# Optimization experiments

Measured on AMD Instinct MI355X. Metric: run time of the kernel, lower is better.

The kernel has to match this reference:

```python
import jax, jax.numpy as jnp
import numpy as np

B, C, H, W = 16, 16, 256, 256
HID, OUT_C, IN_C = 128, 13, 3

_SOBEL_X = np.array([[-1, 0, 1], [-2, 0, 2], [-1, 0, 1]], dtype=np.float32)
_SOBEL_Y = _SOBEL_X.T


def setup_inputs() -> dict:
    key = jax.random.key(0)
    k1, k2, k3, k4 = jax.random.split(key, 4)
    return {
        "input_grid": jax.random.normal(k1, (B, C, H, W), dtype=jnp.float32),
        "w1": jax.random.normal(k2, (HID, 3 * C), dtype=jnp.float32) * 0.0001,
        "b1": jax.random.normal(k3, (HID,), dtype=jnp.float32) * 0.0001,
        "w2": jax.random.normal(k4, (OUT_C, HID), dtype=jnp.float32) * 0.0001,
    }


def _depthwise_sobel(x_padded, filt2d):
    # x_padded: [B, C, H+2, W+2]; depthwise 3x3 valid conv (groups=C)
    c = x_padded.shape[1]
    kern = jnp.broadcast_to(jnp.asarray(filt2d)[None, None], (c, 1, 3, 3))
    return jax.lax.conv_general_dilated(
        x_padded, kern, window_strides=(1, 1), padding="VALID",
        feature_group_count=c,
        dimension_numbers=("NCHW", "OIHW", "NCHW"))


def reference(input_grid, w1, b1, w2):
    # circular pad by 1 on spatial dims
    xp = jnp.pad(input_grid, ((0, 0), (0, 0), (1, 1), (1, 1)), mode="wrap")
    gx = _depthwise_sobel(xp, _SOBEL_X)
    gy = _depthwise_sobel(xp, _SOBEL_Y)
    # perception grid: [B, 3C, H, W]
    perception = jnp.concatenate([input_grid, gx, gy], axis=1)
    # update network: 1x1 conv -> ReLU -> 1x1 conv (dropout = identity in eval)
    h = jax.nn.relu(jnp.einsum("bchw,oc->bohw", perception, w1)
                    + b1[None, :, None, None])
    ds = jnp.einsum("bchw,oc->bohw", h, w2)  # [B, C-IN_C, H, W]
    # residual add to channels 3: of the state
    return input_grid.at[:, IN_C:].add(ds)
```

## Files before the change

kernel.cpp:

```cpp
#include <hip/hip_runtime.h>

#define BB   16
#define CC   16
#define HH   256
#define WW   256
#define HID  128
#define OUTC 13

typedef short short8 __attribute__((ext_vector_type(8)));
typedef float floatx16 __attribute__((ext_vector_type(16)));

__device__ __forceinline__ unsigned short f2bf(float x) {
    unsigned int u = __float_as_uint(x);
    u += 0x7fffu + ((u >> 16) & 1u);
    return (unsigned short)(u >> 16);
}

#define W1F_BYTES 36864
#define W2F_OFF   36864

__global__ __launch_bounds__(256) void gca_prep(
    const float* __restrict__ w1, const float* __restrict__ w2,
    unsigned char* __restrict__ ws)
{
    const int id = blockIdx.x * 256 + threadIdx.x;
    const float SX[9] = {-1.f, 0.f, 1.f, -2.f, 0.f, 2.f, -1.f, 0.f, 1.f};
    const float SY[9] = {-1.f, -2.f, -1.f, 0.f, 0.f, 0.f, 1.f, 2.f, 1.f};

    if (id < 2304) {
        const int mtG  = id / 576;
        const int rem  = id % 576;
        const int tap  = rem / 64;
        const int lane = rem % 64;
        const int p  = lane & 31, hi = lane >> 5;
        const int hid = 32 * mtG + p;
        const float cen = (tap == 4) ? 1.f : 0.f;
        const float sxv = SX[tap], syv = SY[tap];
        const float* wr = w1 + hid * 48;
        unsigned int o[4];
        for (int k = 0; k < 4; ++k) {
            int c0 = 8 * hi + 2 * k;
            float v0 = wr[c0]     * cen + wr[16 + c0]     * sxv + wr[32 + c0]     * syv;
            float v1 = wr[c0 + 1] * cen + wr[16 + c0 + 1] * sxv + wr[32 + c0 + 1] * syv;
            o[k] = (unsigned int)f2bf(v0) | ((unsigned int)f2bf(v1) << 16);
        }
        *(uint4*)(ws + (size_t)id * 16) = make_uint4(o[0], o[1], o[2], o[3]);
    } else if (id < 2816) {
        const int id2 = id - 2304;
        const int s    = id2 / 64;
        const int lane = id2 % 64;
        const int outc = lane & 31, hi = lane >> 5;
        unsigned int o[4];
        for (int k = 0; k < 4; ++k) {
            int hid0 = 16 * s + 8 * hi + 2 * k;
            float v0 = (outc < OUTC) ? w2[outc * HID + hid0]     : 0.f;
            float v1 = (outc < OUTC) ? w2[outc * HID + hid0 + 1] : 0.f;
            o[k] = (unsigned int)f2bf(v0) | ((unsigned int)f2bf(v1) << 16);
        }
        *(uint4*)(ws + W2F_OFF + (size_t)id2 * 16) = make_uint4(o[0], o[1], o[2], o[3]);
    }
}

#define TILE_DW 6120
#define CBUF_DW 2304

__global__ __launch_bounds__(256) void gca_main(
    const float* __restrict__ in,
    const float* __restrict__ b1,
    const unsigned char* __restrict__ ws,
    float* __restrict__ out)
{
    __shared__ unsigned int lds[TILE_DW + CBUF_DW];

    const int tid  = threadIdx.x;
    const int wid  = tid >> 6;
    const int lane = tid & 63;
    const int hw   = wid & 1;
    const int P    = wid >> 1;
    const int p    = lane & 31;
    const int hi   = lane >> 5;

    const int bI = blockIdx.x >> 7;
    const int rm = blockIdx.x & 127;
    const int y0 = (rm >> 3) << 4;
    const int x0 = (rm & 7)  << 5;

    {
        unsigned short* tus = (unsigned short*)lds;
        const float* inb = in + ((size_t)bI << 20);
        for (int i = tid; i < 16 * 18 * 34; i += 256) {
            int c   = i / 612;
            int rem = i % 612;
            int row = rem / 34;
            int col = rem % 34;
            int y = (y0 + row - 1) & 255;
            int x = (x0 + col - 1) & 255;
            float v = inb[(c << 16) + (y << 8) + x];
            tus[(row * 34 + col) * 20 + c] = f2bf(v);
        }
    }
    __syncthreads();

    const unsigned char* w1f = ws + ((size_t)(2 * hw) * 9) * 64 * 16;
    const unsigned char* w2f = ws + W2F_OFF + (size_t)(4 * hw) * 64 * 16;
    const int cb = TILE_DW + P * (64 * 18) + lane * 18;

#pragma unroll 1
    for (int t = 0; t < 8; ++t) {
        const int row = y0 + 2 * t + P;

        floatx16 acc1[2];
#pragma unroll
        for (int m = 0; m < 2; ++m) {
            const int hb = 64 * hw + 32 * m + 4 * hi;
#pragma unroll
            for (int rr = 0; rr < 4; ++rr) {
                float4 bv = *(const float4*)(b1 + hb + 8 * rr);
                acc1[m][4 * rr + 0] = bv.x;
                acc1[m][4 * rr + 1] = bv.y;
                acc1[m][4 * rr + 2] = bv.z;
                acc1[m][4 * rr + 3] = bv.w;
            }
        }

#pragma unroll
        for (int tap = 0; tap < 9; ++tap) {
            const int tr  = 2 * t + P + tap / 3;
            const int col = p + tap % 3;
            const int dwo = (tr * 34 + col) * 10 + 4 * hi;
            union { unsigned int u[4]; short8 s; } bfr;
            uint2 lo2 = *(const uint2*)&lds[dwo];
            uint2 hi2 = *(const uint2*)&lds[dwo + 2];
            bfr.u[0] = lo2.x; bfr.u[1] = lo2.y; bfr.u[2] = hi2.x; bfr.u[3] = hi2.y;
#pragma unroll
            for (int m = 0; m < 2; ++m) {
                short8 af = *(const short8*)(w1f + (size_t)((m * 9 + tap) * 64 + lane) * 16);
                acc1[m] = __builtin_amdgcn_mfma_f32_32x32x16_bf16(af, bfr.s, acc1[m], 0, 0, 0);
            }
        }

        uint2 hrun[8];
#pragma unroll
        for (int m = 0; m < 2; ++m)
#pragma unroll
            for (int rr = 0; rr < 4; ++rr) {
                float h0 = fmaxf(acc1[m][4 * rr + 0], 0.f);
                float h1 = fmaxf(acc1[m][4 * rr + 1], 0.f);
                float h2 = fmaxf(acc1[m][4 * rr + 2], 0.f);
                float h3 = fmaxf(acc1[m][4 * rr + 3], 0.f);
                hrun[4 * m + rr].x = (unsigned int)f2bf(h0) | ((unsigned int)f2bf(h1) << 16);
                hrun[4 * m + rr].y = (unsigned int)f2bf(h2) | ((unsigned int)f2bf(h3) << 16);
            }

        floatx16 acc2 = {};
#pragma unroll
        for (int sp = 0; sp < 4; ++sp) {
            uint2 r0 = hrun[2 * sp];
            uint2 r1 = hrun[2 * sp + 1];
            uint2 x0s, x1s;
            x0s.x = (unsigned int)__shfl_xor((int)r0.x, 32);
            x0s.y = (unsigned int)__shfl_xor((int)r0.y, 32);
            x1s.x = (unsigned int)__shfl_xor((int)r1.x, 32);
            x1s.y = (unsigned int)__shfl_xor((int)r1.y, 32);
            union { unsigned int u[4]; short8 s; } b2;
            uint2 lo = hi ? x1s : r0;
            uint2 hg = hi ? r1  : x0s;
            b2.u[0] = lo.x; b2.u[1] = lo.y; b2.u[2] = hg.x; b2.u[3] = hg.y;
            short8 a2 = *(const short8*)(w2f + (size_t)(sp * 64 + lane) * 16);
            acc2 = __builtin_amdgcn_mfma_f32_32x32x16_bf16(a2, b2.s, acc2, 0, 0, 0);
        }

        if (hw == 1) {
#pragma unroll
            for (int k = 0; k < 8; ++k) {
                uint2 v;
                v.x = __float_as_uint(acc2[2 * k]);
                v.y = __float_as_uint(acc2[2 * k + 1]);
                *(uint2*)&lds[cb + 2 * k] = v;
            }
        }
        __syncthreads();

        if (hw == 0) {
#pragma unroll
            for (int r = 0; r < 16; ++r) {
                int outc = (r & 3) + 8 * (r >> 2) + 4 * hi;
                if (outc < OUTC) {
                    float sum = acc2[r] + __uint_as_float(lds[cb + r]);
                    int idx = ((bI * 16 + 3 + outc) << 16) + (row << 8) + x0 + p;
                    out[idx] = in[idx] + sum;
                }
            }
        } else {
#pragma unroll
            for (int k = 0; k < 2; ++k) {
                int e = lane + 64 * k;
                if (e < 96) {
                    int c  = e >> 5;
                    int px = e & 31;
                    int idx = ((bI * 16 + c) << 16) + (row << 8) + x0 + px;
                    out[idx] = in[idx];
                }
            }
        }
        __syncthreads();
    }
}

extern "C" void kernel_launch(void* const* d_in, const int* in_sizes, int n_in,
                              void* d_out, int out_size, void* d_ws, size_t ws_size,
                              hipStream_t stream) {
    const float* x  = (const float*)d_in[0];
    const float* w1 = (const float*)d_in[1];
    const float* b1 = (const float*)d_in[2];
    const float* w2 = (const float*)d_in[3];
    float* out = (float*)d_out;
    unsigned char* ws = (unsigned char*)d_ws;

    hipLaunchKernelGGL(gca_prep, dim3(11), dim3(256), 0, stream, w1, w2, ws);
    hipLaunchKernelGGL(gca_main, dim3(2048), dim3(256), 0, stream, x, b1, ws, out);
}
```

Before: 214.4 us.

## Give each wave full hidden dimension and shrink tiles to remove cross-wave reduction

Each wave now computes all 128 hidden channels for its row, so the second-layer partial sums no longer have to be exchanged through LDS with two block barriers per row. Tiles shrink from 16 to 8 rows, which halves LDS use and doubles the grid to 4096 blocks, with each wave handling two rows. In exchange, the halo reload fraction goes up (10 rows loaded for 8 output rows), and the doubled accumulator count raises register pressure, which may lower occupancy.

Measured after the change: 260.5 us. +21.5%, slower.

```diff
diff --git a/kernel.cpp b/kernel.cpp
--- a/kernel.cpp
+++ b/kernel.cpp
@@ -16,7 +16,6 @@
     return (unsigned short)(u >> 16);
 }
 
-#define W1F_BYTES 36864
 #define W2F_OFF   36864
 
 __global__ __launch_bounds__(256) void gca_prep(
@@ -61,8 +60,7 @@
     }
 }
 
-#define TILE_DW 6120
-#define CBUF_DW 2304
+#define TILE_DW 3400
 
 __global__ __launch_bounds__(256) void gca_main(
     const float* __restrict__ in,
@@ -70,29 +68,27 @@
     const unsigned char* __restrict__ ws,
     float* __restrict__ out)
 {
-    __shared__ unsigned int lds[TILE_DW + CBUF_DW];
+    __shared__ unsigned int lds[TILE_DW];
 
     const int tid  = threadIdx.x;
     const int wid  = tid >> 6;
     const int lane = tid & 63;
-    const int hw   = wid & 1;
-    const int P    = wid >> 1;
     const int p    = lane & 31;
     const int hi   = lane >> 5;
 
-    const int bI = blockIdx.x >> 7;
-    const int rm = blockIdx.x & 127;
-    const int y0 = (rm >> 3) << 4;
+    const int bI = blockIdx.x >> 8;
+    const int rm = blockIdx.x & 255;
+    const int y0 = (rm >> 3) << 3;
     const int x0 = (rm & 7)  << 5;
 
     {
         unsigned short* tus = (unsigned short*)lds;
         const float* inb = in + ((size_t)bI << 20);
-        for (int i = tid; i < 16 * 18 * 34; i += 256) {
-            int c   = i / 612;
-            int rem = i % 612;
-            int row = rem / 34;
-            int col = rem % 34;
+        for (int i = tid; i < 16 * 10 * 34; i += 256) {
+            int col = i % 34;
+            int rem = i / 34;
+            int row = rem % 10;
+            int c   = rem / 10;
             int y = (y0 + row - 1) & 255;
             int x = (x0 + col - 1) & 255;
             float v = inb[(c << 16) + (y << 8) + x];
@@ -101,31 +97,26 @@
     }
     __syncthreads();
 
-    const unsigned char* w1f = ws + ((size_t)(2 * hw) * 9) * 64 * 16;
-    const unsigned char* w2f = ws + W2F_OFF + (size_t)(4 * hw) * 64 * 16;
-    const int cb = TILE_DW + P * (64 * 18) + lane * 18;
+#pragma unroll 1
+    for (int rr2 = 0; rr2 < 2; ++rr2) {
+        const int r   = 2 * wid + rr2;
+        const int row = y0 + r;
 
-#pragma unroll 1
-    for (int t = 0; t < 8; ++t) {
-        const int row = y0 + 2 * t + P;
-
-        floatx16 acc1[2];
+        floatx16 acc1[4];
 #pragma unroll
-        for (int m = 0; m < 2; ++m) {
-            const int hb = 64 * hw + 32 * m + 4 * hi;
+        for (int mt = 0; mt < 4; ++mt)
 #pragma unroll
-            for (int rr = 0; rr < 4; ++rr) {
-                float4 bv = *(const float4*)(b1 + hb + 8 * rr);
-                acc1[m][4 * rr + 0] = bv.x;
-                acc1[m][4 * rr + 1] = bv.y;
-                acc1[m][4 * rr + 2] = bv.z;
-                acc1[m][4 * rr + 3] = bv.w;
+            for (int q = 0; q < 4; ++q) {
+                float4 bv = *(const float4*)(b1 + 32 * mt + 8 * q + 4 * hi);
+                acc1[mt][4 * q + 0] = bv.x;
+                acc1[mt][4 * q + 1] = bv.y;
+                acc1[mt][4 * q + 2] = bv.z;
+                acc1[mt][4 * q + 3] = bv.w;
             }
-        }
 
 #pragma unroll
         for (int tap = 0; tap < 9; ++tap) {
-            const int tr  = 2 * t + P + tap / 3;
+            const int tr  = r + tap / 3;
             const int col = p + tap % 3;
             const int dwo = (tr * 34 + col) * 10 + 4 * hi;
             union { unsigned int u[4]; short8 s; } bfr;
@@ -133,77 +124,60 @@
             uint2 hi2 = *(const uint2*)&lds[dwo + 2];
             bfr.u[0] = lo2.x; bfr.u[1] = lo2.y; bfr.u[2] = hi2.x; bfr.u[3] = hi2.y;
 #pragma unroll
-            for (int m = 0; m < 2; ++m) {
-                short8 af = *(const short8*)(w1f + (size_t)((m * 9 + tap) * 64 + lane) * 16);
-                acc1[m] = __builtin_amdgcn_mfma_f32_32x32x16_bf16(af, bfr.s, acc1[m], 0, 0, 0);
+            for (int mt = 0; mt < 4; ++mt) {
+                short8 af = *(const short8*)(ws + (size_t)((mt * 9 + tap) * 64 + lane) * 16);
+                acc1[mt] = __builtin_amdgcn_mfma_f32_32x32x16_bf16(af, bfr.s, acc1[mt], 0, 0, 0);
             }
         }
 
-        uint2 hrun[8];
+        uint2 hrun[16];
 #pragma unroll
-        for (int m = 0; m < 2; ++m)
+        for (int mt = 0; mt < 4; ++mt)
 #pragma unroll
-            for (int rr = 0; rr < 4; ++rr) {
-                float h0 = fmaxf(acc1[m][4 * rr + 0], 0.f);
-                float h1 = fmaxf(acc1[m][4 * rr + 1], 0.f);
-                float h2 = fmaxf(acc1[m][4 * rr + 2], 0.f);
-                float h3 = fmaxf(acc1[m][4 * rr + 3], 0.f);
-                hrun[4 * m + rr].x = (unsigned int)f2bf(h0) | ((unsigned int)f2bf(h1) << 16);
-                hrun[4 * m + rr].y = (unsigned int)f2bf(h2) | ((unsigned int)f2bf(h3) << 16);
+            for (int q = 0; q < 4; ++q) {
+                float h0 = fmaxf(acc1[mt][4 * q + 0], 0.f);
+                float h1 = fmaxf(acc1[mt][4 * q + 1], 0.f);
+                float h2 = fmaxf(acc1[mt][4 * q + 2], 0.f);
+                float h3 = fmaxf(acc1[mt][4 * q + 3], 0.f);
+                hrun[4 * mt + q].x = (unsigned int)f2bf(h0) | ((unsigned int)f2bf(h1) << 16);
+                hrun[4 * mt + q].y = (unsigned int)f2bf(h2) | ((unsigned int)f2bf(h3) << 16);
             }
 
         floatx16 acc2 = {};
 #pragma unroll
-        for (int sp = 0; sp < 4; ++sp) {
-            uint2 r0 = hrun[2 * sp];
-            uint2 r1 = hrun[2 * sp + 1];
+        for (int s = 0; s < 8; ++s) {
+            uint2 r0 = hrun[2 * s];
+            uint2 r1 = hrun[2 * s + 1];
             uint2 x0s, x1s;
             x0s.x = (unsigned int)__shfl_xor((int)r0.x, 32);
             x0s.y = (unsigned int)__shfl_xor((int)r0.y, 32);
             x1s.x = (unsigned int)__shfl_xor((int)r1.x, 32);
             x1s.y = (unsigned int)__shfl_xor((int)r1.y, 32);
-            union { unsigned int u[4]; short8 s; } b2;
+            union { unsigned int u[4]; short8 s8; } b2;
             uint2 lo = hi ? x1s : r0;
             uint2 hg = hi ? r1  : x0s;
             b2.u[0] = lo.x; b2.u[1] = lo.y; b2.u[2] = hg.x; b2.u[3] = hg.y;
-            short8 a2 = *(const short8*)(w2f + (size_t)(sp * 64 + lane) * 16);
-            acc2 = __builtin_amdgcn_mfma_f32_32x32x16_bf16(a2, b2.s, acc2, 0, 0, 0);
+            short8 a2 = *(const short8*)(ws + W2F_OFF + (size_t)(s * 64 + lane) * 16);
+            acc2 = __builtin_amdgcn_mfma_f32_32x32x16_bf16(a2, b2.s8, acc2, 0, 0, 0);
         }
 
-        if (hw == 1) {
 #pragma unroll
-            for (int k = 0; k < 8; ++k) {
-                uint2 v;
-                v.x = __float_as_uint(acc2[2 * k]);
-                v.y = __float_as_uint(acc2[2 * k + 1]);
-                *(uint2*)&lds[cb + 2 * k] = v;
+        for (int reg = 0; reg < 16; ++reg) {
+            int oc = (reg & 3) + 8 * (reg >> 2) + 4 * hi;
+            if (oc < OUTC) {
+                int idx = ((bI * 16 + 3 + oc) << 16) + (row << 8) + x0 + p;
+                out[idx] = in[idx] + acc2[reg];
             }
         }
-        __syncthreads();
-
-        if (hw == 0) {
-#pragma unroll
-            for (int r = 0; r < 16; ++r) {
-                int outc = (r & 3) + 8 * (r >> 2) + 4 * hi;
-                if (outc < OUTC) {
-                    float sum = acc2[r] + __uint_as_float(lds[cb + r]);
-                    int idx = ((bI * 16 + 3 + outc) << 16) + (row << 8) + x0 + p;
-                    out[idx] = in[idx] + sum;
-                }
-            }
-        } else {
-#pragma unroll
-            for (int k = 0; k < 2; ++k) {
-                int e = lane + 64 * k;
-                if (e < 96) {
-                    int c  = e >> 5;
-                    int px = e & 31;
-                    int idx = ((bI * 16 + c) << 16) + (row << 8) + x0 + px;
-                    out[idx] = in[idx];
-                }
+        {
+            int c  = lane >> 5;
+            int idx = ((bI * 16 + c) << 16) + (row << 8) + x0 + p;
+            out[idx] = in[idx];
+            if (lane < 32) {
+                int idx2 = ((bI * 16 + 2) << 16) + (row << 8) + x0 + lane;
+                out[idx2] = in[idx2];
             }
         }
-        __syncthreads();
     }
 }
 
@@ -218,5 +192,5 @@
     unsigned char* ws = (unsigned char*)d_ws;
 
     hipLaunchKernelGGL(gca_prep, dim3(11), dim3(256), 0, stream, w1, w2, ws);
-    hipLaunchKernelGGL(gca_main, dim3(2048), dim3(256), 0, stream, x, b1, ws, out);
+    hipLaunchKernelGGL(gca_main, dim3(4096), dim3(256), 0, stream, x, b1, ws, out);
 }
```
